# Optimization experiments

Measured on AMD Instinct MI355X. Metric: run time of the kernel, lower is better.

## Reference

```python
import jax, jax.numpy as jnp
import numpy as np

B, C, H, W = 4, 256, 64, 64
D = C // 8  # query/key projection dim


def setup_inputs() -> dict:
    key = jax.random.key(0)
    ks = jax.random.split(key, 8)
    s = 0.02
    return {
        "x": jax.random.normal(ks[0], (B, C, H, W), dtype=jnp.float32),
        "Wq": jax.random.normal(ks[1], (D, C), dtype=jnp.float32) * s,
        "bq": jax.random.normal(ks[2], (D,), dtype=jnp.float32) * s,
        "Wk": jax.random.normal(ks[3], (D, C), dtype=jnp.float32) * s,
        "bk": jax.random.normal(ks[4], (D,), dtype=jnp.float32) * s,
        "Wv": jax.random.normal(ks[5], (C, C), dtype=jnp.float32) * s,
        "bv": jax.random.normal(ks[6], (C,), dtype=jnp.float32) * s,
        "gamma": jax.random.normal(ks[7], (1,), dtype=jnp.float32),
    }


def reference(x, Wq, bq, Wk, bk, Wv, bv, gamma):
    b, c, h, w = x.shape
    n = h * w
    xf = x.reshape(b, c, n)                                  # B,C,N
    # 1x1 convs == per-pixel linear projections
    q = jnp.einsum("dc,bcn->bdn", Wq, xf) + bq[None, :, None]  # B,D,N
    k = jnp.einsum("dc,bcn->bdn", Wk, xf) + bk[None, :, None]  # B,D,N
    v = jnp.einsum("ec,bcn->ben", Wv, xf) + bv[None, :, None]  # B,C,N
    # energy[b,i,j] = <q[:, i], k[:, j]>  (query index i, key index j)
    energy = jnp.einsum("bdi,bdj->bij", q, k)                # B,N,N
    attention = jax.nn.softmax(energy, axis=-1)              # softmax over keys j
    # out[b,c,i] = sum_j v[b,c,j] * attention[b,i,j]
    out = jnp.einsum("bcj,bij->bci", v, attention)           # B,C,N
    out = out.reshape(b, c, h, w)
    return gamma[0] * out + x
```

## Files before the change

kernel.cpp:

```cpp
#include <hip/hip_runtime.h>
#include <hip/hip_bf16.h>
#include <cstdint>

#define B_ 4
#define C_ 256
#define N_ 4096
#define D_ 32

typedef __attribute__((ext_vector_type(8))) short bf16x8;
typedef __attribute__((ext_vector_type(4))) short s16x4;
typedef __attribute__((ext_vector_type(4))) float f32x4;

__device__ inline unsigned short f2bf(float f) {
    union { float f; uint32_t u; } v; v.f = f;
    uint32_t u = v.u;
    u += 0x7FFFu + ((u >> 16) & 1u);
    return (unsigned short)(u >> 16);
}

__global__ __launch_bounds__(256) void proj_kernel(
    const float* __restrict__ x,
    const float* __restrict__ Wq, const float* __restrict__ bq,
    const float* __restrict__ Wk, const float* __restrict__ bk,
    const float* __restrict__ Wv, const float* __restrict__ bv,
    unsigned short* __restrict__ Qt, unsigned short* __restrict__ Kt,
    unsigned short* __restrict__ V)
{
    __shared__ __align__(16) char smem[73728];
    const int t  = threadIdx.x;
    const int w  = t >> 6;
    const int l  = t & 63;
    const int lg = l >> 4;
    const int ll = l & 15;
    const int n0 = blockIdx.x * 64;
    const int b  = blockIdx.y;

    #pragma unroll
    for (int rep = 0; rep < 16; ++rep) {
        int flat = rep * 256 + t;
        int c = flat >> 4, chunk = flat & 15;
        f32x4 xv = *reinterpret_cast<const f32x4*>(
            x + ((size_t)(b * C_ + c)) * N_ + n0 + chunk * 4);
        #pragma unroll
        for (int j = 0; j < 4; ++j) {
            int n = chunk * 4 + j;
            *reinterpret_cast<unsigned short*>(
                smem + n * 512 + ((c * 2) ^ ((n & 7) << 4))) = f2bf(xv[j]);
        }
    }

    auto stageW = [&](int kc, int bufsel) {
        char* Wb = smem + 32768 + bufsel * 20480;
        #pragma unroll
        for (int rep = 0; rep < 10; ++rep) {
            int flat = rep * 256 + t;
            int r = flat >> 3, kl = (flat & 7) * 4;
            const float* src;
            if (r < 32)      src = Wq + r * C_ + kc * 32 + kl;
            else if (r < 64) src = Wk + (r - 32) * C_ + kc * 32 + kl;
            else             src = Wv + (r - 64) * C_ + kc * 32 + kl;
            f32x4 wv = *reinterpret_cast<const f32x4*>(src);
            s16x4 pk;
            #pragma unroll
            for (int j = 0; j < 4; ++j) pk[j] = (short)f2bf(wv[j]);
            *reinterpret_cast<s16x4*>(Wb + r * 64 + ((kl * 2) ^ ((r & 3) << 4))) = pk;
        }
    };

    stageW(0, 0);
    __syncthreads();

    f32x4 acc[5][4];
    #pragma unroll
    for (int rt = 0; rt < 5; ++rt)
        #pragma unroll
        for (int nt = 0; nt < 4; ++nt) acc[rt][nt] = (f32x4){0.f, 0.f, 0.f, 0.f};

    for (int kc = 0; kc < 8; ++kc) {
        const int buf = kc & 1;
        if (kc < 7) stageW(kc + 1, buf ^ 1);
        char* Wb = smem + 32768 + buf * 20480;
        bf16x8 Af[5], Bf[4];
        #pragma unroll
        for (int rt = 0; rt < 5; ++rt) {
            int r = w * 80 + rt * 16 + ll;
            Af[rt] = *reinterpret_cast<const bf16x8*>(
                Wb + r * 64 + ((lg * 16) ^ ((r & 3) << 4)));
        }
        #pragma unroll
        for (int nt = 0; nt < 4; ++nt) {
            int n = nt * 16 + ll;
            Bf[nt] = *reinterpret_cast<const bf16x8*>(
                smem + n * 512 + ((kc * 64 + lg * 16) ^ ((n & 7) << 4)));
        }
        #pragma unroll
        for (int rt = 0; rt < 5; ++rt)
            #pragma unroll
            for (int nt = 0; nt < 4; ++nt)
                acc[rt][nt] = __builtin_amdgcn_mfma_f32_16x16x32_bf16(
                    Af[rt], Bf[nt], acc[rt][nt], 0, 0, 0);
        __syncthreads();
    }

    #pragma unroll
    for (int rt = 0; rt < 5; ++rt) {
        const int rrow = w * 80 + rt * 16 + lg * 4;
        float bias[4];
        #pragma unroll
        for (int q = 0; q < 4; ++q) {
            int rg = rrow + q;
            bias[q] = (rg < 32) ? bq[rg] : (rg < 64) ? bk[rg - 32] : bv[rg - 64];
        }
        if (rrow < 64) {
            const int d0 = rrow & 31;
            unsigned short* dst = (rrow < 32) ? Qt : Kt;
            #pragma unroll
            for (int nt = 0; nt < 4; ++nt) {
                int n = n0 + nt * 16 + ll;
                s16x4 sv;
                #pragma unroll
                for (int q = 0; q < 4; ++q)
                    sv[q] = (short)f2bf(acc[rt][nt][q] + bias[q]);
                *reinterpret_cast<s16x4*>(dst + ((size_t)b * N_ + n) * D_ + d0) = sv;
            }
        } else {
            #pragma unroll
            for (int nt = 0; nt < 4; ++nt) {
                int n = n0 + nt * 16 + ll;
                #pragma unroll
                for (int q = 0; q < 4; ++q) {
                    int c = rrow - 64 + q;
                    V[((size_t)(b * C_ + c)) * N_ + n] = f2bf(acc[rt][nt][q] + bias[q]);
                }
            }
        }
    }
}

__device__ inline void stageV(const unsigned short* __restrict__ Vg, int b, int j0,
                              char* VsBuf, int w, int l) {
    #pragma unroll
    for (int i = 0; i < 4; ++i) {
        const int Lbyte = i * 8192 + w * 1024 + l * 16;
        const int c   = Lbyte >> 7;
        const int off = Lbyte & 127;
        const int src_off = off ^ ((c & 7) << 4);
        const unsigned short* src = Vg + ((size_t)(b * C_ + c)) * N_ + j0 + (src_off >> 1);
        char* dst = VsBuf + i * 8192 + w * 1024;
        __builtin_amdgcn_global_load_lds(
            (const __attribute__((address_space(1))) uint32_t*)src,
            (__attribute__((address_space(3))) uint32_t*)dst, 16, 0, 0);
    }
}

__global__ __launch_bounds__(512) void attn_kernel(
    const unsigned short* __restrict__ Qt, const unsigned short* __restrict__ Kt,
    const unsigned short* __restrict__ Vg, const float* __restrict__ x,
    const float* __restrict__ gamma, float* __restrict__ out)
{
    __shared__ __align__(16) char smem[82432];
    char* Pbase = smem + 65536;
    float* LbufF = reinterpret_cast<float*>(smem + 81920);
    const int t  = threadIdx.x;
    const int w  = t >> 6;
    const int l  = t & 63;
    const int lg = l >> 4;
    const int ll = l & 15;
    const int qg = w >> 2;
    const int ch = w & 3;
    const int qr = w >> 1;
    const int jcb = (w & 1) * 2;
    const int n0 = blockIdx.x * 64;
    const int b  = blockIdx.y;

    const bf16x8 qfrag = *reinterpret_cast<const bf16x8*>(
        Qt + ((size_t)b * N_ + n0 + qr * 16 + ll) * D_ + 8 * lg);

    f32x4 acc[2][4];
    #pragma unroll
    for (int qt = 0; qt < 2; ++qt)
        #pragma unroll
        for (int ct = 0; ct < 4; ++ct) acc[qt][ct] = (f32x4){0.f, 0.f, 0.f, 0.f};
    float l_lane[4] = {0.f, 0.f, 0.f, 0.f};

    stageV(Vg, b, 0, smem, w, l);
    bf16x8 kcur[2], knxt[2];
    #pragma unroll
    for (int s = 0; s < 2; ++s)
        kcur[s] = *reinterpret_cast<const bf16x8*>(
            Kt + ((size_t)b * N_ + (jcb + s) * 16 + ll) * D_ + 8 * lg);

    const f32x4 zero4 = {0.f, 0.f, 0.f, 0.f};

    for (int kt = 0; kt < 64; ++kt) {
        const int buf = kt & 1;
        const int ktn = (kt < 63) ? kt + 1 : 63;

        #pragma unroll
        for (int s = 0; s < 2; ++s)
            knxt[s] = *reinterpret_cast<const bf16x8*>(
                Kt + ((size_t)b * N_ + ktn * 64 + (jcb + s) * 16 + ll) * D_ + 8 * lg);

        f32x4 sf[2];
        #pragma unroll
        for (int s = 0; s < 2; ++s)
            sf[s] = __builtin_amdgcn_mfma_f32_16x16x32_bf16(qfrag, kcur[s], zero4, 0, 0, 0);

        float pv[2][4];
        #pragma unroll
        for (int s = 0; s < 2; ++s)
            #pragma unroll
            for (int r = 0; r < 4; ++r) {
                float p = __expf(fminf(sf[s][r], 60.f));
                pv[s][r] = p;
                l_lane[r] += p;
            }

        if (kt < 63)
            stageV(Vg, b, ktn * 64, smem + ((kt + 1) & 1) * 32768, w, l);

        char* Pw = Pbase + buf * 8192;
        #pragma unroll
        for (int s = 0; s < 2; ++s)
            #pragma unroll
            for (int r = 0; r < 4; ++r) {
                int row = qr * 16 + lg * 4 + r;
                int col = (jcb + s) * 16 + ll;
                *reinterpret_cast<unsigned short*>(
                    Pw + row * 128 + ((col * 2) ^ ((row & 7) << 4))) = f2bf(pv[s][r]);
            }

        asm volatile("s_waitcnt lgkmcnt(0)" ::: "memory");
        asm volatile("s_waitcnt vmcnt(6)" ::: "memory");
        __builtin_amdgcn_s_barrier();
        asm volatile("" ::: "memory");

        char* Pr = Pbase + buf * 8192;
        bf16x8 pfrag[2][2];
        #pragma unroll
        for (int qt = 0; qt < 2; ++qt)
            #pragma unroll
            for (int kh = 0; kh < 2; ++kh) {
                int row = qg * 32 + qt * 16 + ll;
                pfrag[qt][kh] = *reinterpret_cast<const bf16x8*>(
                    Pr + row * 128 + ((kh * 64 + lg * 16) ^ ((row & 7) << 4)));
            }
        char* Vs = smem + buf * 32768;
        #pragma unroll
        for (int ct = 0; ct < 4; ++ct) {
            int c = ch * 64 + ct * 16 + ll;
            #pragma unroll
            for (int kh = 0; kh < 2; ++kh) {
                bf16x8 vf = *reinterpret_cast<const bf16x8*>(
                    Vs + c * 128 + ((kh * 64 + lg * 16) ^ ((c & 7) << 4)));
                #pragma unroll
                for (int qt = 0; qt < 2; ++qt)
                    acc[qt][ct] = __builtin_amdgcn_mfma_f32_16x16x32_bf16(
                        pfrag[qt][kh], vf, acc[qt][ct], 0, 0, 0);
            }
        }

        #pragma unroll
        for (int s = 0; s < 2; ++s) kcur[s] = knxt[s];
    }

    #pragma unroll
    for (int off = 1; off < 16; off <<= 1)
        #pragma unroll
        for (int r = 0; r < 4; ++r)
            l_lane[r] += __shfl_xor(l_lane[r], off);
    if (ll == 0) {
        #pragma unroll
        for (int r = 0; r < 4; ++r) LbufF[w * 16 + lg * 4 + r] = l_lane[r];
    }
    __syncthreads();

    float inv[2][4];
    #pragma unroll
    for (int qt = 0; qt < 2; ++qt)
        #pragma unroll
        for (int r = 0; r < 4; ++r) {
            int qrow = qg * 2 + qt;
            int lq = lg * 4 + r;
            float ls = LbufF[(2 * qrow) * 16 + lq] + LbufF[(2 * qrow + 1) * 16 + lq];
            inv[qt][r] = 1.f / ls;
        }

    #pragma unroll
    for (int qt = 0; qt < 2; ++qt)
        #pragma unroll
        for (int ct = 0; ct < 4; ++ct) {
            int c = ch * 64 + ct * 16 + ll;
            int ncol = qg * 32 + qt * 16 + lg * 4;
            f32x4 v;
            #pragma unroll
            for (int r = 0; r < 4; ++r) v[r] = acc[qt][ct][r] * inv[qt][r];
            *reinterpret_cast<f32x4*>(smem + c * 256 + ((ncol * 4) ^ ((c & 7) << 4))) = v;
        }
    __syncthreads();

    const float g0 = gamma[0];
    #pragma unroll
    for (int p = 0; p < 8; ++p) {
        int li = p * 512 + t;
        int c  = li >> 4;
        int n4 = (li & 15) * 4;
        f32x4 ov = *reinterpret_cast<const f32x4*>(
            smem + c * 256 + ((n4 * 4) ^ ((c & 7) << 4)));
        size_t gi = ((size_t)(b * C_ + c)) * N_ + n0 + n4;
        f32x4 xv = *reinterpret_cast<const f32x4*>(x + gi);
        f32x4 res;
        #pragma unroll
        for (int j = 0; j < 4; ++j) res[j] = g0 * ov[j] + xv[j];
        *reinterpret_cast<f32x4*>(out + gi) = res;
    }
}

extern "C" void kernel_launch(void* const* d_in, const int* in_sizes, int n_in,
                              void* d_out, int out_size, void* d_ws, size_t ws_size,
                              hipStream_t stream) {
    const float* x     = (const float*)d_in[0];
    const float* Wq    = (const float*)d_in[1];
    const float* bq    = (const float*)d_in[2];
    const float* Wk    = (const float*)d_in[3];
    const float* bk    = (const float*)d_in[4];
    const float* Wv    = (const float*)d_in[5];
    const float* bv    = (const float*)d_in[6];
    const float* gamma = (const float*)d_in[7];
    float* out = (float*)d_out;

    char* ws = (char*)d_ws;
    unsigned short* Qt = (unsigned short*)(ws);
    unsigned short* Kt = (unsigned short*)(ws + (1u << 20));
    unsigned short* V  = (unsigned short*)(ws + (2u << 20));

    proj_kernel<<<dim3(N_ / 64, B_), 256, 0, stream>>>(
        x, Wq, bq, Wk, bk, Wv, bv, Qt, Kt, V);
    attn_kernel<<<dim3(N_ / 64, B_), 512, 0, stream>>>(
        Qt, Kt, V, x, gamma, out);
}
```

Measured before the change: 170.7 us.

## Split attention blocks by channel half, pre-convert weights to bf16

The attention grid doubles so each block handles 128 of the 256 output channels, halving V staging and LDS use. The intent is higher occupancy and more blocks to fill the GPU. The cost is that QK^T and softmax are recomputed twice per query tile. A separate kernel converts the weights to bf16 once, and the projection kernel now reads its A fragments straight from global memory, which removes the LDS weight staging and the per-iteration barrier. The V prefetch is moved after the barrier and the vmcnt wait is adjusted to match.

After: 161.5 us. -5.4%, faster.

```diff
diff --git a/kernel.cpp b/kernel.cpp
--- a/kernel.cpp
+++ b/kernel.cpp
@@ -18,15 +18,30 @@
     return (unsigned short)(u >> 16);
 }
 
+__global__ __launch_bounds__(256) void wconv_kernel(
+    const float* __restrict__ Wq, const float* __restrict__ Wk,
+    const float* __restrict__ Wv, unsigned short* __restrict__ Wb)
+{
+    int i = (blockIdx.x * 256 + threadIdx.x) * 4;
+    int r = i >> 8, k = i & 255;
+    const float* src = (r < 32) ? Wq + r * 256 + k
+                     : (r < 64) ? Wk + (r - 32) * 256 + k
+                                : Wv + (r - 64) * 256 + k;
+    f32x4 v = *reinterpret_cast<const f32x4*>(src);
+    s16x4 o;
+    #pragma unroll
+    for (int j = 0; j < 4; ++j) o[j] = (short)f2bf(v[j]);
+    *reinterpret_cast<s16x4*>(Wb + i) = o;
+}
+
 __global__ __launch_bounds__(256) void proj_kernel(
-    const float* __restrict__ x,
-    const float* __restrict__ Wq, const float* __restrict__ bq,
-    const float* __restrict__ Wk, const float* __restrict__ bk,
-    const float* __restrict__ Wv, const float* __restrict__ bv,
+    const float* __restrict__ x, const unsigned short* __restrict__ Wb,
+    const float* __restrict__ bq, const float* __restrict__ bk,
+    const float* __restrict__ bv,
     unsigned short* __restrict__ Qt, unsigned short* __restrict__ Kt,
     unsigned short* __restrict__ V)
 {
-    __shared__ __align__(16) char smem[73728];
+    __shared__ __align__(16) char smem[32768];
     const int t  = threadIdx.x;
     const int w  = t >> 6;
     const int l  = t & 63;
@@ -49,44 +64,31 @@
         }
     }
 
-    auto stageW = [&](int kc, int bufsel) {
-        char* Wb = smem + 32768 + bufsel * 20480;
-        #pragma unroll
-        for (int rep = 0; rep < 10; ++rep) {
-            int flat = rep * 256 + t;
-            int r = flat >> 3, kl = (flat & 7) * 4;
-            const float* src;
-            if (r < 32)      src = Wq + r * C_ + kc * 32 + kl;
-            else if (r < 64) src = Wk + (r - 32) * C_ + kc * 32 + kl;
-            else             src = Wv + (r - 64) * C_ + kc * 32 + kl;
-            f32x4 wv = *reinterpret_cast<const f32x4*>(src);
-            s16x4 pk;
-            #pragma unroll
-            for (int j = 0; j < 4; ++j) pk[j] = (short)f2bf(wv[j]);
-            *reinterpret_cast<s16x4*>(Wb + r * 64 + ((kl * 2) ^ ((r & 3) << 4))) = pk;
-        }
-    };
-
-    stageW(0, 0);
+    bf16x8 Af[5], Afn[5];
+    #pragma unroll
+    for (int rt = 0; rt < 5; ++rt) {
+        int r = w * 80 + rt * 16 + ll;
+        Af[rt] = *reinterpret_cast<const bf16x8*>(Wb + r * 256 + lg * 8);
+    }
+
+    f32x4 acc[5][4];
+    #pragma unroll
+    for (int rt = 0; rt < 5; ++rt)
+        #pragma unroll
+        for (int nt = 0; nt < 4; ++nt) acc[rt][nt] = (f32x4){0.f, 0.f, 0.f, 0.f};
+
     __syncthreads();
 
-    f32x4 acc[5][4];
-    #pragma unroll
-    for (int rt = 0; rt < 5; ++rt)
-        #pragma unroll
-        for (int nt = 0; nt < 4; ++nt) acc[rt][nt] = (f32x4){0.f, 0.f, 0.f, 0.f};
-
     for (int kc = 0; kc < 8; ++kc) {
-        const int buf = kc & 1;
-        if (kc < 7) stageW(kc + 1, buf ^ 1);
-        char* Wb = smem + 32768 + buf * 20480;
-        bf16x8 Af[5], Bf[4];
-        #pragma unroll
-        for (int rt = 0; rt < 5; ++rt) {
-            int r = w * 80 + rt * 16 + ll;
-            Af[rt] = *reinterpret_cast<const bf16x8*>(
-                Wb + r * 64 + ((lg * 16) ^ ((r & 3) << 4)));
-        }
+        if (kc < 7) {
+            #pragma unroll
+            for (int rt = 0; rt < 5; ++rt) {
+                int r = w * 80 + rt * 16 + ll;
+                Afn[rt] = *reinterpret_cast<const bf16x8*>(
+                    Wb + r * 256 + (kc + 1) * 32 + lg * 8);
+            }
+        }
+        bf16x8 Bf[4];
         #pragma unroll
         for (int nt = 0; nt < 4; ++nt) {
             int n = nt * 16 + ll;
@@ -99,7 +101,10 @@
             for (int nt = 0; nt < 4; ++nt)
                 acc[rt][nt] = __builtin_amdgcn_mfma_f32_16x16x32_bf16(
                     Af[rt], Bf[nt], acc[rt][nt], 0, 0, 0);
-        __syncthreads();
+        if (kc < 7) {
+            #pragma unroll
+            for (int rt = 0; rt < 5; ++rt) Af[rt] = Afn[rt];
+        }
     }
 
     #pragma unroll
@@ -137,15 +142,16 @@
     }
 }
 
-__device__ inline void stageV(const unsigned short* __restrict__ Vg, int b, int j0,
-                              char* VsBuf, int w, int l) {
-    #pragma unroll
-    for (int i = 0; i < 4; ++i) {
+__device__ inline void stageV(const unsigned short* __restrict__ Vg, int b,
+                              int c0, int j0, char* VsBuf, int w, int l) {
+    #pragma unroll
+    for (int i = 0; i < 2; ++i) {
         const int Lbyte = i * 8192 + w * 1024 + l * 16;
         const int c   = Lbyte >> 7;
         const int off = Lbyte & 127;
         const int src_off = off ^ ((c & 7) << 4);
-        const unsigned short* src = Vg + ((size_t)(b * C_ + c)) * N_ + j0 + (src_off >> 1);
+        const unsigned short* src =
+            Vg + ((size_t)(b * C_ + c0 + c)) * N_ + j0 + (src_off >> 1);
         char* dst = VsBuf + i * 8192 + w * 1024;
         __builtin_amdgcn_global_load_lds(
             (const __attribute__((address_space(1))) uint32_t*)src,
@@ -158,9 +164,9 @@
     const unsigned short* __restrict__ Vg, const float* __restrict__ x,
     const float* __restrict__ gamma, float* __restrict__ out)
 {
-    __shared__ __align__(16) char smem[82432];
-    char* Pbase = smem + 65536;
-    float* LbufF = reinterpret_cast<float*>(smem + 81920);
+    __shared__ __align__(16) char smem[49664];
+    char* Pbase = smem + 32768;
+    float* LbufF = reinterpret_cast<float*>(smem + 49152);
     const int t  = threadIdx.x;
     const int w  = t >> 6;
     const int l  = t & 63;
@@ -170,20 +176,21 @@
     const int ch = w & 3;
     const int qr = w >> 1;
     const int jcb = (w & 1) * 2;
-    const int n0 = blockIdx.x * 64;
+    const int n0 = (blockIdx.x >> 1) * 64;
+    const int c0 = (blockIdx.x & 1) * 128;
     const int b  = blockIdx.y;
 
     const bf16x8 qfrag = *reinterpret_cast<const bf16x8*>(
         Qt + ((size_t)b * N_ + n0 + qr * 16 + ll) * D_ + 8 * lg);
 
-    f32x4 acc[2][4];
+    f32x4 acc[2][2];
     #pragma unroll
     for (int qt = 0; qt < 2; ++qt)
         #pragma unroll
-        for (int ct = 0; ct < 4; ++ct) acc[qt][ct] = (f32x4){0.f, 0.f, 0.f, 0.f};
+        for (int ct = 0; ct < 2; ++ct) acc[qt][ct] = (f32x4){0.f, 0.f, 0.f, 0.f};
     float l_lane[4] = {0.f, 0.f, 0.f, 0.f};
 
-    stageV(Vg, b, 0, smem, w, l);
+    stageV(Vg, b, c0, 0, smem, w, l);
     bf16x8 kcur[2], knxt[2];
     #pragma unroll
     for (int s = 0; s < 2; ++s)
@@ -215,9 +222,6 @@
                 pv[s][r] = p;
                 l_lane[r] += p;
             }
-
-        if (kt < 63)
-            stageV(Vg, b, ktn * 64, smem + ((kt + 1) & 1) * 32768, w, l);
 
         char* Pw = Pbase + buf * 8192;
         #pragma unroll
@@ -231,9 +235,12 @@
             }
 
         asm volatile("s_waitcnt lgkmcnt(0)" ::: "memory");
-        asm volatile("s_waitcnt vmcnt(6)" ::: "memory");
+        asm volatile("s_waitcnt vmcnt(2)" ::: "memory");
         __builtin_amdgcn_s_barrier();
         asm volatile("" ::: "memory");
+
+        if (kt < 63)
+            stageV(Vg, b, c0, ktn * 64, smem + (buf ^ 1) * 16384, w, l);
 
         char* Pr = Pbase + buf * 8192;
         bf16x8 pfrag[2][2];
@@ -245,14 +252,14 @@
                 pfrag[qt][kh] = *reinterpret_cast<const bf16x8*>(
                     Pr + row * 128 + ((kh * 64 + lg * 16) ^ ((row & 7) << 4)));
             }
-        char* Vs = smem + buf * 32768;
-        #pragma unroll
-        for (int ct = 0; ct < 4; ++ct) {
-            int c = ch * 64 + ct * 16 + ll;
+        char* Vs = smem + buf * 16384;
+        #pragma unroll
+        for (int ct = 0; ct < 2; ++ct) {
+            int cl = ch * 32 + ct * 16 + ll;
             #pragma unroll
             for (int kh = 0; kh < 2; ++kh) {
                 bf16x8 vf = *reinterpret_cast<const bf16x8*>(
-                    Vs + c * 128 + ((kh * 64 + lg * 16) ^ ((c & 7) << 4)));
+                    Vs + cl * 128 + ((kh * 64 + lg * 16) ^ ((cl & 7) << 4)));
                 #pragma unroll
                 for (int qt = 0; qt < 2; ++qt)
                     acc[qt][ct] = __builtin_amdgcn_mfma_f32_16x16x32_bf16(
@@ -289,25 +296,25 @@
     #pragma unroll
     for (int qt = 0; qt < 2; ++qt)
         #pragma unroll
-        for (int ct = 0; ct < 4; ++ct) {
-            int c = ch * 64 + ct * 16 + ll;
+        for (int ct = 0; ct < 2; ++ct) {
+            int cl = ch * 32 + ct * 16 + ll;
             int ncol = qg * 32 + qt * 16 + lg * 4;
             f32x4 v;
             #pragma unroll
             for (int r = 0; r < 4; ++r) v[r] = acc[qt][ct][r] * inv[qt][r];
-            *reinterpret_cast<f32x4*>(smem + c * 256 + ((ncol * 4) ^ ((c & 7) << 4))) = v;
+            *reinterpret_cast<f32x4*>(smem + cl * 256 + ((ncol * 4) ^ ((cl & 7) << 4))) = v;
         }
     __syncthreads();
 
     const float g0 = gamma[0];
     #pragma unroll
-    for (int p = 0; p < 8; ++p) {
+    for (int p = 0; p < 4; ++p) {
         int li = p * 512 + t;
-        int c  = li >> 4;
+        int cl = li >> 4;
         int n4 = (li & 15) * 4;
         f32x4 ov = *reinterpret_cast<const f32x4*>(
-            smem + c * 256 + ((n4 * 4) ^ ((c & 7) << 4)));
-        size_t gi = ((size_t)(b * C_ + c)) * N_ + n0 + n4;
+            smem + cl * 256 + ((n4 * 4) ^ ((cl & 7) << 4)));
+        size_t gi = ((size_t)(b * C_ + c0 + cl)) * N_ + n0 + n4;
         f32x4 xv = *reinterpret_cast<const f32x4*>(x + gi);
         f32x4 res;
         #pragma unroll
@@ -333,9 +340,11 @@
     unsigned short* Qt = (unsigned short*)(ws);
     unsigned short* Kt = (unsigned short*)(ws + (1u << 20));
     unsigned short* V  = (unsigned short*)(ws + (2u << 20));
-
+    unsigned short* Wb = (unsigned short*)(ws + (10u << 20));
+
+    wconv_kernel<<<dim3(80), 256, 0, stream>>>(Wq, Wk, Wv, Wb);
     proj_kernel<<<dim3(N_ / 64, B_), 256, 0, stream>>>(
-        x, Wq, bq, Wk, bk, Wv, bv, Qt, Kt, V);
-    attn_kernel<<<dim3(N_ / 64, B_), 512, 0, stream>>>(
+        x, Wb, bq, bk, bv, Qt, Kt, V);
+    attn_kernel<<<dim3(2 * N_ / 64, B_), 512, 0, stream>>>(
         Qt, Kt, V, x, gamma, out);
 }
```
